# Performance work log

Hardware: AMD Instinct MI355X
Metric: run time of the kernel (lower is better)

Reference implementation:

```python
import jax, jax.numpy as jnp
import numpy as np

V, E, H, B, S = 50000, 512, 1024, 256, 256


def setup_inputs() -> dict:
    key = jax.random.key(0)
    ks = jax.random.split(key, 8)
    inputs = jax.random.randint(ks[0], (B, S), 0, V)
    emb = jax.random.normal(ks[1], (V, E), dtype=jnp.float32)
    sx, sh = 1.0 / np.sqrt(E), 1.0 / np.sqrt(H)  # ~orthogonal column scale
    Wx_f = jax.random.normal(ks[2], (E, 4 * H), dtype=jnp.float32) * sx
    Wh_f = jax.random.normal(ks[3], (H, 4 * H), dtype=jnp.float32) * sh
    Wx_b = jax.random.normal(ks[4], (E, 4 * H), dtype=jnp.float32) * sx
    Wh_b = jax.random.normal(ks[5], (H, 4 * H), dtype=jnp.float32) * sh
    # gate order i, f, o, c ; forget-gate bias initialized to 1 as in the source
    bias = jnp.concatenate([jnp.zeros(H), jnp.ones(H), jnp.zeros(H), jnp.zeros(H)]).astype(jnp.float32)
    W_hq = jax.random.normal(ks[6], (H, 10), dtype=jnp.float32) * sh
    b_q = jnp.zeros(10, dtype=jnp.float32)
    return {"inputs": inputs, "emb": emb, "Wx_f": Wx_f, "Wh_f": Wh_f, "b_f": bias,
            "Wx_b": Wx_b, "Wh_b": Wh_b, "b_b": bias, "W_hq": W_hq, "b_q": b_q}


def _lstm_final_h(x_tbe, Wx, Wh, b):
    """x_tbe: [S,B,E] time-major. Returns final hidden state [B,H]."""
    h0 = jnp.zeros((x_tbe.shape[1], H), dtype=x_tbe.dtype)
    c0 = jnp.zeros_like(h0)

    def cell(carry, X):
        h, c = carry
        g = X @ Wx + h @ Wh + b          # [B, 4H] fused gate pre-activations
        i, f, o, ct = jnp.split(g, 4, axis=-1)
        c = jax.nn.sigmoid(f) * c + jax.nn.sigmoid(i) * jnp.tanh(ct)
        h = jax.nn.sigmoid(o) * jnp.tanh(c)
        return (h, c), None

    (h, _), _ = jax.lax.scan(cell, (h0, c0), x_tbe)
    return h


def reference(inputs, emb, Wx_f, Wh_f, b_f, Wx_b, Wh_b, b_b, W_hq, b_q):
    x = emb[inputs]                      # [B,S,E]
    x = jnp.transpose(x, (1, 0, 2))      # [S,B,E] time-major
    h_fwd = _lstm_final_h(x, Wx_f, Wh_f, b_f)
    h_bwd = _lstm_final_h(x[::-1], Wx_b, Wh_b, b_b)
    logits = (h_fwd + h_bwd) @ W_hq + b_q
    return jax.nn.softmax(logits, axis=1)
```

## Files before the change

kernel.cpp:

```cpp
#include <hip/hip_runtime.h>

#define S_LEN 256
#define BATCH 256
#define EDIM 512
#define HDIM 1024
#define LDS_BYTES 131072

typedef short short8 __attribute__((ext_vector_type(8)));
typedef float f32x4 __attribute__((ext_vector_type(4)));
typedef unsigned long long u64;
typedef unsigned short us;

__device__ __forceinline__ us f2bf(float f) {
  unsigned u = __float_as_uint(f);
  u = u + 0x7FFFu + ((u >> 16) & 1u);
  return (us)(u >> 16);
}
__device__ __forceinline__ float bf2f(us s) {
  return __uint_as_float(((unsigned)s) << 16);
}
__device__ __forceinline__ float sigf(float x) { return 1.0f / (1.0f + __expf(-x)); }
__device__ __forceinline__ float tanh_(float x) { return 2.0f / (1.0f + __expf(-2.0f * x)) - 1.0f; }

#define MFMA(d, a, b) d = __builtin_amdgcn_mfma_f32_16x16x32_bf16(a, b, d, 0, 0, 0)

__device__ __forceinline__ short8 load_hfrag(const us* p) {
  union { u64 d[2]; short8 v; } u;
  u.d[0] = __hip_atomic_load((const u64*)p,       __ATOMIC_RELAXED, __HIP_MEMORY_SCOPE_AGENT);
  u.d[1] = __hip_atomic_load((const u64*)(p + 4), __ATOMIC_RELAXED, __HIP_MEMORY_SCOPE_AGENT);
  return u.v;
}
__device__ __forceinline__ short8 ldf(const us* p) {
  union { uint4 d; short8 v; } u;
  u.d = *(const uint4*)p;
  return u.v;
}


__global__ void gather_embed(const int* __restrict__ inputs, const float* __restrict__ emb,
                             us* __restrict__ Xf) {
  int T = blockIdx.x * 256 + threadIdx.x;
  int kt = T & 15;
  int b  = (T >> 4) & 255;
  int s  = T >> 12;
  int vid = inputs[b * S_LEN + s];
  const float* src = emb + (size_t)vid * EDIM + kt * 32;
  int c = b & 15;
  us* ub = Xf + ((size_t)(s * 16 + kt) * 16 + (b >> 4)) * 512;
#pragma unroll
  for (int q = 0; q < 4; ++q) {
    float4 v0 = *(const float4*)(src + q * 8);
    float4 v1 = *(const float4*)(src + q * 8 + 4);
    us o[8] = { f2bf(v0.x), f2bf(v0.y), f2bf(v0.z), f2bf(v0.w),
                f2bf(v1.x), f2bf(v1.y), f2bf(v1.z), f2bf(v1.w) };
    *(uint4*)(ub + (size_t)(c + 16 * q) * 8) = *(const uint4*)o;
  }
}

__global__ void pack_w(const float* __restrict__ Wx_f, const float* __restrict__ Wh_f,
                       const float* __restrict__ Wx_b, const float* __restrict__ Wh_b,
                       us* __restrict__ Wxp, us* __restrict__ Whp) {
  int T = blockIdx.x * 256 + threadIdx.x;
  int c = T & 15;
  int q = (T >> 4) & 3;
  int t = (T >> 6) & 7;
  int r = T >> 9;
  int kit = r % 48;
  int jbd = r / 48;
  int jb  = jbd & 31;
  int dir = jbd >> 5;
  int g = t >> 1, h16 = t & 1;
  int n = g * 1024 + jb * 32 + h16 * 16 + c;
  const float* W; int k0;
  if (kit < 16) { W = dir ? Wx_b : Wx_f; k0 = kit * 32 + q * 8; }
  else          { W = dir ? Wh_b : Wh_f; k0 = (kit - 16) * 32 + q * 8; }
  us o[8];
#pragma unroll
  for (int e = 0; e < 8; ++e) o[e] = f2bf(W[(size_t)(k0 + e) * 4096 + n]);
  us* dst;
  if (kit < 16) dst = Wxp + (((size_t)(dir * 32 + jb) * 16 + kit) * 8 + t) * 512;
  else          dst = Whp + (((size_t)(dir * 32 + jb) * 32 + (kit - 16)) * 8 + t) * 512;
  *(uint4*)(dst + (size_t)(c + 16 * q) * 8) = *(const uint4*)o;
}

__global__ __launch_bounds__(256, 1) void lstm_main(
    const us* __restrict__ Xf,
    const us* __restrict__ Wxp,
    const us* __restrict__ Whp,
    const float* __restrict__ bias_f,
    const float* __restrict__ bias_b,
    us* __restrict__ Hf,
    unsigned int* __restrict__ slots)
{
  extern __shared__ __align__(16) unsigned char smem[];

  const int bx   = blockIdx.x;
  const int xcd  = bx & 7;
  const int dir  = xcd >> 2;
  const int joct = xcd & 3;
  const int rr   = bx >> 3;
  const int jb   = joct * 8 + (rr & 7);
  const int mq   = rr >> 3;

  const int tid  = threadIdx.x;
  const int wave = tid >> 6;
  const int lane = tid & 63;
  const int mw   = wave & 1;
  const int nw   = wave >> 1;
  const int c    = lane & 15;
  const int q    = lane >> 4;
  const int lofs = lane * 8;

  {
    const uint4* src = (const uint4*)(Whp + (((size_t)(dir * 32 + jb) * 32 + 16) * 8) * 512);
    for (int i = tid; i < 8192; i += 256) *(uint4*)(smem + (size_t)i * 16) = src[i];
  }
  const float* bias = dir ? bias_b : bias_f;
  const int j = jb * 32 + nw * 16 + c;
  float bg[4];
#pragma unroll
  for (int g = 0; g < 4; ++g) bg[g] = bias[g * HDIM + j];
  __syncthreads();

  unsigned int* grp_slots = slots + (dir * 4 + mq) * (32 * 16);
  unsigned int* my_slot   = grp_slots + jb * 16;

  const int bt0 = mq * 4 + mw * 2;
  const us* xu_base  = Xf + (size_t)bt0 * 512 + lofs;
  const us* wxu = Wxp + (((size_t)(dir * 32 + jb) * 16) * 8 + nw) * 512 + lofs;
  const us* whu = Whp + (((size_t)(dir * 32 + jb) * 32) * 8 + nw) * 512 + lofs;
  const int ldsofs = (nw * 512 + lane * 8) * 2;

  float c_reg[2][4] = {{0.f,0.f,0.f,0.f},{0.f,0.f,0.f,0.f}};

  for (int s = 0; s < S_LEN; ++s) {
    const int sx = dir ? (S_LEN - 1 - s) : s;
    const int p  = s & 1;

    f32x4 acc[2][4];
#pragma unroll
    for (int mt = 0; mt < 2; ++mt)
#pragma unroll
      for (int g = 0; g < 4; ++g)
        acc[mt][g] = (f32x4){bg[g], bg[g], bg[g], bg[g]};

    {
      const us* xu = xu_base + (size_t)sx * (16 * 16 * 512);
#pragma unroll 4
      for (int k = 0; k < 16; ++k) {
        short8 a0 = ldf(xu + (size_t)k * 8192);
        short8 a1 = ldf(xu + (size_t)k * 8192 + 512);
        const us* wb = wxu + (size_t)k * 4096;
        short8 b0 = ldf(wb);
        short8 b1 = ldf(wb + 1024);
        short8 b2 = ldf(wb + 2048);
        short8 b3 = ldf(wb + 3072);
        MFMA(acc[0][0], a0, b0); MFMA(acc[0][1], a0, b1);
        MFMA(acc[0][2], a0, b2); MFMA(acc[0][3], a0, b3);
        MFMA(acc[1][0], a1, b0); MFMA(acc[1][1], a1, b1);
        MFMA(acc[1][2], a1, b2); MFMA(acc[1][3], a1, b3);
      }
    }

    if (s > 0) {
      if (tid < 32) {
        const unsigned int* sl = grp_slots + tid * 16;
        for (;;) {
          unsigned v = __hip_atomic_load(sl, __ATOMIC_RELAXED, __HIP_MEMORY_SCOPE_AGENT);
          if (!__any(v < (unsigned)s)) break;
          __builtin_amdgcn_s_sleep(1);
        }
      }
      __syncthreads();
      asm volatile("" ::: "memory");
    }

    {
      const us* hu = Hf + (((size_t)(p * 2 + dir) * 32) * 16 + bt0) * 512 + lofs;
      short8 pa0[4], pa1[4];
#pragma unroll
      for (int i = 0; i < 4; ++i) {
        pa0[i] = load_hfrag(hu + (size_t)i * 8192);
        pa1[i] = load_hfrag(hu + (size_t)i * 8192 + 512);
      }
#pragma unroll 4
      for (int k = 0; k < 16; ++k) {
        short8 a0 = pa0[k & 3], a1 = pa1[k & 3];
        pa0[k & 3] = load_hfrag(hu + (size_t)(k + 4) * 8192);
        pa1[k & 3] = load_hfrag(hu + (size_t)(k + 4) * 8192 + 512);
        const us* wb = whu + (size_t)k * 4096;
        short8 b0 = ldf(wb);
        short8 b1 = ldf(wb + 1024);
        short8 b2 = ldf(wb + 2048);
        short8 b3 = ldf(wb + 3072);
        MFMA(acc[0][0], a0, b0); MFMA(acc[0][1], a0, b1);
        MFMA(acc[0][2], a0, b2); MFMA(acc[0][3], a0, b3);
        MFMA(acc[1][0], a1, b0); MFMA(acc[1][1], a1, b1);
        MFMA(acc[1][2], a1, b2); MFMA(acc[1][3], a1, b3);
      }
#pragma unroll 4
      for (int k = 16; k < 28; ++k) {
        short8 a0 = pa0[k & 3], a1 = pa1[k & 3];
        pa0[k & 3] = load_hfrag(hu + (size_t)(k + 4) * 8192);
        pa1[k & 3] = load_hfrag(hu + (size_t)(k + 4) * 8192 + 512);
        const unsigned char* lb = smem + (size_t)(k - 16) * 8192 + ldsofs;
        short8 b0 = *(const short8*)(lb);
        short8 b1 = *(const short8*)(lb + 2048);
        short8 b2 = *(const short8*)(lb + 4096);
        short8 b3 = *(const short8*)(lb + 6144);
        MFMA(acc[0][0], a0, b0); MFMA(acc[0][1], a0, b1);
        MFMA(acc[0][2], a0, b2); MFMA(acc[0][3], a0, b3);
        MFMA(acc[1][0], a1, b0); MFMA(acc[1][1], a1, b1);
        MFMA(acc[1][2], a1, b2); MFMA(acc[1][3], a1, b3);
      }
#pragma unroll
      for (int k = 28; k < 32; ++k) {
        short8 a0 = pa0[k & 3], a1 = pa1[k & 3];
        const unsigned char* lb = smem + (size_t)(k - 16) * 8192 + ldsofs;
        short8 b0 = *(const short8*)(lb);
        short8 b1 = *(const short8*)(lb + 2048);
        short8 b2 = *(const short8*)(lb + 4096);
        short8 b3 = *(const short8*)(lb + 6144);
        MFMA(acc[0][0], a0, b0); MFMA(acc[0][1], a0, b1);
        MFMA(acc[0][2], a0, b2); MFMA(acc[0][3], a0, b3);
        MFMA(acc[1][0], a1, b0); MFMA(acc[1][1], a1, b1);
        MFMA(acc[1][2], a1, b2); MFMA(acc[1][3], a1, b3);
      }
    }

    {
      const int q2 = nw * 2 + (c >> 3);
      const int e2 = c & 7;
      const size_t ob = ((size_t)(((p ^ 1) * 2 + dir) * 32 + jb) * 16 + bt0) * 512;
#pragma unroll
      for (int mt = 0; mt < 2; ++mt) {
        us* hd = Hf + ob + (size_t)mt * 512 + (size_t)(16 * q2) * 8 + e2;
#pragma unroll
        for (int rg = 0; rg < 4; ++rg) {
          float gi = acc[mt][0][rg], gf = acc[mt][1][rg];
          float go = acc[mt][2][rg], gc = acc[mt][3][rg];
          float cn = sigf(gf) * c_reg[mt][rg] + sigf(gi) * tanh_(gc);
          c_reg[mt][rg] = cn;
          __hip_atomic_store(hd + (size_t)(q * 4 + rg) * 8, f2bf(sigf(go) * tanh_(cn)),
                             __ATOMIC_RELAXED, __HIP_MEMORY_SCOPE_AGENT);
        }
      }
    }
    asm volatile("s_waitcnt vmcnt(0)" ::: "memory");
    __syncthreads();
    if (tid == 0)
      __hip_atomic_store(my_slot, (unsigned)(s + 1), __ATOMIC_RELAXED, __HIP_MEMORY_SCOPE_AGENT);
  }
}

__global__ void final_softmax(const us* __restrict__ Hf,
                              const float* __restrict__ Whq,
                              const float* __restrict__ bq,
                              float* __restrict__ out) {
  __shared__ float red[4][10];
  const int b = blockIdx.x;
  const int tid = threadIdx.x;
  float acc[10];
#pragma unroll
  for (int qq = 0; qq < 10; ++qq) acc[qq] = 0.f;
#pragma unroll
  for (int u = 0; u < 4; ++u) {
    int j = tid * 4 + u;
    int kt = j >> 5, q2 = (j & 31) >> 3, e = j & 7;
    size_t idx = (((size_t)kt * 16 + (b >> 4)) * 512) + ((size_t)((b & 15) + 16 * q2)) * 8 + e;
    float xv = bf2f(Hf[idx]) + bf2f(Hf[(size_t)32 * 16 * 512 + idx]);
#pragma unroll
    for (int qq = 0; qq < 10; ++qq) acc[qq] += xv * Whq[j * 10 + qq];
  }
#pragma unroll
  for (int qq = 0; qq < 10; ++qq)
#pragma unroll
    for (int off = 32; off; off >>= 1) acc[qq] += __shfl_down(acc[qq], off, 64);
  if ((tid & 63) == 0)
#pragma unroll
    for (int qq = 0; qq < 10; ++qq) red[tid >> 6][qq] = acc[qq];
  __syncthreads();
  if (tid == 0) {
    float t[10];
#pragma unroll
    for (int qq = 0; qq < 10; ++qq)
      t[qq] = red[0][qq] + red[1][qq] + red[2][qq] + red[3][qq] + bq[qq];
    float mx = t[0];
#pragma unroll
    for (int qq = 1; qq < 10; ++qq) mx = fmaxf(mx, t[qq]);
    float sum = 0.f;
#pragma unroll
    for (int qq = 0; qq < 10; ++qq) { t[qq] = __expf(t[qq] - mx); sum += t[qq]; }
    float inv = 1.0f / sum;
#pragma unroll
    for (int qq = 0; qq < 10; ++qq) out[b * 10 + qq] = t[qq] * inv;
  }
}

extern "C" void kernel_launch(void* const* d_in, const int* in_sizes, int n_in,
                              void* d_out, int out_size, void* d_ws, size_t ws_size,
                              hipStream_t stream) {
  const int*   inputs = (const int*)d_in[0];
  const float* emb    = (const float*)d_in[1];
  const float* Wx_f   = (const float*)d_in[2];
  const float* Wh_f   = (const float*)d_in[3];
  const float* b_f    = (const float*)d_in[4];
  const float* Wx_b   = (const float*)d_in[5];
  const float* Wh_b   = (const float*)d_in[6];
  const float* b_b    = (const float*)d_in[7];
  const float* W_hq   = (const float*)d_in[8];
  const float* b_q    = (const float*)d_in[9];
  float* out = (float*)d_out;

  char* ws = (char*)d_ws;
  us* Xf  = (us*)ws;
  us* Wxp = (us*)(ws + (64ull << 20));
  us* Whp = (us*)(ws + (72ull << 20));
  us* Hf  = (us*)(ws + (88ull << 20));
  unsigned int* slt = (unsigned int*)(ws + (90ull << 20));

  hipMemsetAsync(Hf, 0, (size_t)2 * 2 * 32 * 16 * 512 * sizeof(us), stream);
  hipMemsetAsync(slt, 0, 8 * 32 * 16 * sizeof(unsigned int), stream);

  gather_embed<<<4096, 256, 0, stream>>>(inputs, emb, Xf);
  pack_w<<<6144, 256, 0, stream>>>(Wx_f, Wh_f, Wx_b, Wh_b, Wxp, Whp);

  hipFuncSetAttribute((const void*)lstm_main,
                      hipFuncAttributeMaxDynamicSharedMemorySize, LDS_BYTES);

  const us* xf_p = Xf;
  const us* wxp_p = Wxp;
  const us* whp_p = Whp;
  const float* bf_p = b_f;
  const float* bb_p = b_b;
  us* hf_p = Hf;
  unsigned int* slt_p = slt;
  void* kargs[] = { (void*)&xf_p, (void*)&wxp_p, (void*)&whp_p, (void*)&bf_p,
                    (void*)&bb_p, (void*)&hf_p, (void*)&slt_p };
  hipLaunchCooperativeKernel((void*)lstm_main, dim3(256), dim3(256), kargs, LDS_BYTES, stream);

  final_softmax<<<256, 256, 0, stream>>>(Hf, W_hq, b_q, out);
}
```

Measured before the change: 4.606 ms.

## Double waves per block so each wave handles one batch M-tile

Changes the persistent LSTM kernel from 256 to 512 threads per block, splitting the M dimension across four waves instead of two, so each wave computes one 16-row tile rather than two. This halves per-wave serial MFMA work and register use each timestep and adds latency hiding through more waves per CU. In exchange, each weight B-fragment (global and LDS) is now loaded by twice as many waves, raising memory and LDS traffic, and the block-wide barrier covers more waves.

```diff
diff --git a/kernel.cpp b/kernel.cpp
--- a/kernel.cpp
+++ b/kernel.cpp
@@ -83,7 +83,7 @@
   *(uint4*)(dst + (size_t)(c + 16 * q) * 8) = *(const uint4*)o;
 }
 
-__global__ __launch_bounds__(256, 1) void lstm_main(
+__global__ __launch_bounds__(512, 1) void lstm_main(
     const us* __restrict__ Xf,
     const us* __restrict__ Wxp,
     const us* __restrict__ Whp,
@@ -105,15 +105,15 @@
   const int tid  = threadIdx.x;
   const int wave = tid >> 6;
   const int lane = tid & 63;
-  const int mw   = wave & 1;
-  const int nw   = wave >> 1;
+  const int mw   = wave & 3;
+  const int nw   = wave >> 2;
   const int c    = lane & 15;
   const int q    = lane >> 4;
   const int lofs = lane * 8;
 
   {
     const uint4* src = (const uint4*)(Whp + (((size_t)(dir * 32 + jb) * 32 + 16) * 8) * 512);
-    for (int i = tid; i < 8192; i += 256) *(uint4*)(smem + (size_t)i * 16) = src[i];
+    for (int i = tid; i < 8192; i += 512) *(uint4*)(smem + (size_t)i * 16) = src[i];
   }
   const float* bias = dir ? bias_b : bias_f;
   const int j = jb * 32 + nw * 16 + c;
@@ -125,40 +125,35 @@
   unsigned int* grp_slots = slots + (dir * 4 + mq) * (32 * 16);
   unsigned int* my_slot   = grp_slots + jb * 16;
 
-  const int bt0 = mq * 4 + mw * 2;
+  const int bt0 = mq * 4 + mw;
   const us* xu_base  = Xf + (size_t)bt0 * 512 + lofs;
   const us* wxu = Wxp + (((size_t)(dir * 32 + jb) * 16) * 8 + nw) * 512 + lofs;
   const us* whu = Whp + (((size_t)(dir * 32 + jb) * 32) * 8 + nw) * 512 + lofs;
   const int ldsofs = (nw * 512 + lane * 8) * 2;
 
-  float c_reg[2][4] = {{0.f,0.f,0.f,0.f},{0.f,0.f,0.f,0.f}};
+  float c_reg[4] = {0.f, 0.f, 0.f, 0.f};
 
   for (int s = 0; s < S_LEN; ++s) {
     const int sx = dir ? (S_LEN - 1 - s) : s;
     const int p  = s & 1;
 
-    f32x4 acc[2][4];
-#pragma unroll
-    for (int mt = 0; mt < 2; ++mt)
-#pragma unroll
-      for (int g = 0; g < 4; ++g)
-        acc[mt][g] = (f32x4){bg[g], bg[g], bg[g], bg[g]};
+    f32x4 acc[4];
+#pragma unroll
+    for (int g = 0; g < 4; ++g)
+      acc[g] = (f32x4){bg[g], bg[g], bg[g], bg[g]};
 
     {
       const us* xu = xu_base + (size_t)sx * (16 * 16 * 512);
 #pragma unroll 4
       for (int k = 0; k < 16; ++k) {
         short8 a0 = ldf(xu + (size_t)k * 8192);
-        short8 a1 = ldf(xu + (size_t)k * 8192 + 512);
         const us* wb = wxu + (size_t)k * 4096;
         short8 b0 = ldf(wb);
         short8 b1 = ldf(wb + 1024);
         short8 b2 = ldf(wb + 2048);
         short8 b3 = ldf(wb + 3072);
-        MFMA(acc[0][0], a0, b0); MFMA(acc[0][1], a0, b1);
-        MFMA(acc[0][2], a0, b2); MFMA(acc[0][3], a0, b3);
-        MFMA(acc[1][0], a1, b0); MFMA(acc[1][1], a1, b1);
-        MFMA(acc[1][2], a1, b2); MFMA(acc[1][3], a1, b3);
+        MFMA(acc[0], a0, b0); MFMA(acc[1], a0, b1);
+        MFMA(acc[2], a0, b2); MFMA(acc[3], a0, b3);
       }
     }
 
@@ -177,54 +172,43 @@
 
     {
       const us* hu = Hf + (((size_t)(p * 2 + dir) * 32) * 16 + bt0) * 512 + lofs;
-      short8 pa0[4], pa1[4];
-#pragma unroll
-      for (int i = 0; i < 4; ++i) {
-        pa0[i] = load_hfrag(hu + (size_t)i * 8192);
-        pa1[i] = load_hfrag(hu + (size_t)i * 8192 + 512);
-      }
+      short8 pa[4];
+#pragma unroll
+      for (int i = 0; i < 4; ++i) pa[i] = load_hfrag(hu + (size_t)i * 8192);
 #pragma unroll 4
       for (int k = 0; k < 16; ++k) {
-        short8 a0 = pa0[k & 3], a1 = pa1[k & 3];
-        pa0[k & 3] = load_hfrag(hu + (size_t)(k + 4) * 8192);
-        pa1[k & 3] = load_hfrag(hu + (size_t)(k + 4) * 8192 + 512);
+        short8 a0 = pa[k & 3];
+        pa[k & 3] = load_hfrag(hu + (size_t)(k + 4) * 8192);
         const us* wb = whu + (size_t)k * 4096;
         short8 b0 = ldf(wb);
         short8 b1 = ldf(wb + 1024);
         short8 b2 = ldf(wb + 2048);
         short8 b3 = ldf(wb + 3072);
-        MFMA(acc[0][0], a0, b0); MFMA(acc[0][1], a0, b1);
-        MFMA(acc[0][2], a0, b2); MFMA(acc[0][3], a0, b3);
-        MFMA(acc[1][0], a1, b0); MFMA(acc[1][1], a1, b1);
-        MFMA(acc[1][2], a1, b2); MFMA(acc[1][3], a1, b3);
+        MFMA(acc[0], a0, b0); MFMA(acc[1], a0, b1);
+        MFMA(acc[2], a0, b2); MFMA(acc[3], a0, b3);
       }
 #pragma unroll 4
       for (int k = 16; k < 28; ++k) {
-        short8 a0 = pa0[k & 3], a1 = pa1[k & 3];
-        pa0[k & 3] = load_hfrag(hu + (size_t)(k + 4) * 8192);
-        pa1[k & 3] = load_hfrag(hu + (size_t)(k + 4) * 8192 + 512);
+        short8 a0 = pa[k & 3];
+        pa[k & 3] = load_hfrag(hu + (size_t)(k + 4) * 8192);
         const unsigned char* lb = smem + (size_t)(k - 16) * 8192 + ldsofs;
         short8 b0 = *(const short8*)(lb);
         short8 b1 = *(const short8*)(lb + 2048);
         short8 b2 = *(const short8*)(lb + 4096);
         short8 b3 = *(const short8*)(lb + 6144);
-        MFMA(acc[0][0], a0, b0); MFMA(acc[0][1], a0, b1);
-        MFMA(acc[0][2], a0, b2); MFMA(acc[0][3], a0, b3);
-        MFMA(acc[1][0], a1, b0); MFMA(acc[1][1], a1, b1);
-        MFMA(acc[1][2], a1, b2); MFMA(acc[1][3], a1, b3);
+        MFMA(acc[0], a0, b0); MFMA(acc[1], a0, b1);
+        MFMA(acc[2], a0, b2); MFMA(acc[3], a0, b3);
       }
 #pragma unroll
       for (int k = 28; k < 32; ++k) {
-        short8 a0 = pa0[k & 3], a1 = pa1[k & 3];
+        short8 a0 = pa[k & 3];
         const unsigned char* lb = smem + (size_t)(k - 16) * 8192 + ldsofs;
         short8 b0 = *(const short8*)(lb);
         short8 b1 = *(const short8*)(lb + 2048);
         short8 b2 = *(const short8*)(lb + 4096);
         short8 b3 = *(const short8*)(lb + 6144);
-        MFMA(acc[0][0], a0, b0); MFMA(acc[0][1], a0, b1);
-        MFMA(acc[0][2], a0, b2); MFMA(acc[0][3], a0, b3);
-        MFMA(acc[1][0], a1, b0); MFMA(acc[1][1], a1, b1);
-        MFMA(acc[1][2], a1, b2); MFMA(acc[1][3], a1, b3);
+        MFMA(acc[0], a0, b0); MFMA(acc[1], a0, b1);
+        MFMA(acc[2], a0, b2); MFMA(acc[3], a0, b3);
       }
     }
 
@@ -232,18 +216,15 @@
       const int q2 = nw * 2 + (c >> 3);
       const int e2 = c & 7;
       const size_t ob = ((size_t)(((p ^ 1) * 2 + dir) * 32 + jb) * 16 + bt0) * 512;
-#pragma unroll
-      for (int mt = 0; mt < 2; ++mt) {
-        us* hd = Hf + ob + (size_t)mt * 512 + (size_t)(16 * q2) * 8 + e2;
-#pragma unroll
-        for (int rg = 0; rg < 4; ++rg) {
-          float gi = acc[mt][0][rg], gf = acc[mt][1][rg];
-          float go = acc[mt][2][rg], gc = acc[mt][3][rg];
-          float cn = sigf(gf) * c_reg[mt][rg] + sigf(gi) * tanh_(gc);
-          c_reg[mt][rg] = cn;
-          __hip_atomic_store(hd + (size_t)(q * 4 + rg) * 8, f2bf(sigf(go) * tanh_(cn)),
-                             __ATOMIC_RELAXED, __HIP_MEMORY_SCOPE_AGENT);
-        }
+      us* hd = Hf + ob + (size_t)(16 * q2) * 8 + e2;
+#pragma unroll
+      for (int rg = 0; rg < 4; ++rg) {
+        float gi = acc[0][rg], gf = acc[1][rg];
+        float go = acc[2][rg], gc = acc[3][rg];
+        float cn = sigf(gf) * c_reg[rg] + sigf(gi) * tanh_(gc);
+        c_reg[rg] = cn;
+        __hip_atomic_store(hd + (size_t)(q * 4 + rg) * 8, f2bf(sigf(go) * tanh_(cn)),
+                           __ATOMIC_RELAXED, __HIP_MEMORY_SCOPE_AGENT);
       }
     }
     asm volatile("s_waitcnt vmcnt(0)" ::: "memory");
@@ -337,7 +318,7 @@
   unsigned int* slt_p = slt;
   void* kargs[] = { (void*)&xf_p, (void*)&wxp_p, (void*)&whp_p, (void*)&bf_p,
                     (void*)&bb_p, (void*)&hf_p, (void*)&slt_p };
-  hipLaunchCooperativeKernel((void*)lstm_main, dim3(256), dim3(256), kargs, LDS_BYTES, stream);
+  hipLaunchCooperativeKernel((void*)lstm_main, dim3(256), dim3(512), kargs, LDS_BYTES, stream);
 
   final_softmax<<<256, 256, 0, stream>>>(Hf, W_hq, b_q, out);
 }
```

Result: slower. 4.714 ms (+2.4%).
